# Kernel optimization log

Measured on AMD Instinct MI355X. Metric: run time of the kernel, lower is better.

## Reference

```python
import jax, jax.numpy as jnp
import numpy as np

N = 50000      # nodes
E = 800000     # edges (before self loops)
F_IN = 50      # PPI num_features
H = 4          # heads
C = 64         # hidden per head
NC = 121       # PPI num_classes
NEG_SLOPE = 0.2


def setup_inputs() -> dict:
    key = jax.random.key(0)
    ks = jax.random.split(key, 20)
    p = lambda k, shape: (jax.random.normal(k, shape, jnp.float32) * 0.1)
    x0 = jax.random.normal(ks[0], (N, F_IN), jnp.float32)
    edge_index = jax.random.randint(ks[1], (2, E), 0, N, dtype=jnp.int64)
    return dict(
        x0=x0, edge_index=edge_index,
        W1=p(ks[2], (F_IN, H * C)), as1=p(ks[3], (H, C)), ad1=p(ks[4], (H, C)),
        res1=p(ks[5], (F_IN, H * C)), b1=jnp.zeros((H * C,), jnp.float32),
        W2=p(ks[6], (H * C, H * C)), as2=p(ks[7], (H, C)), ad2=p(ks[8], (H, C)),
        res2=p(ks[9], (H * C, H * C)), b2=jnp.zeros((H * C,), jnp.float32),
        W3=p(ks[10], (H * C, H * NC)), as3=p(ks[11], (H, NC)), ad3=p(ks[12], (H, NC)),
        res3=p(ks[13], (H * C, NC)), b3=jnp.zeros((NC,), jnp.float32),
    )


def _gat(x, src, dst, W, a_src, a_dst, resW, b, concat):
    """PyG-style GATConv with residual, self loops already in (src, dst)."""
    n = x.shape[0]
    heads, outc = a_src.shape
    h = (x @ W).reshape(n, heads, outc)                 # [N,H,C]
    al_s = (h * a_src).sum(-1)                          # [N,H]
    al_d = (h * a_dst).sum(-1)                          # [N,H]
    e = jax.nn.leaky_relu(al_s[src] + al_d[dst], NEG_SLOPE)  # [E,H]
    m = jax.ops.segment_max(e, dst, num_segments=n)     # stable softmax per dst
    ex = jnp.exp(e - m[dst])
    denom = jax.ops.segment_sum(ex, dst, num_segments=n)
    alpha = ex / denom[dst]                             # [E,H]
    out = jax.ops.segment_sum(h[src] * alpha[:, :, None], dst, num_segments=n)  # [N,H,C]
    out = out.reshape(n, heads * outc) if concat else out.mean(axis=1)
    return out + x @ resW + b


def reference(x0, edge_index,
              W1, as1, ad1, res1, b1,
              W2, as2, ad2, res2, b2,
              W3, as3, ad3, res3, b3):
    n = x0.shape[0]
    loop = jnp.arange(n, dtype=edge_index.dtype)        # add self loops (PyG default)
    src = jnp.concatenate([edge_index[0], loop])
    dst = jnp.concatenate([edge_index[1], loop])
    x1 = jax.nn.relu(_gat(x0, src, dst, W1, as1, ad1, res1, b1, True))
    x2 = jax.nn.relu(_gat(x1, src, dst, W2, as2, ad2, res2, b2, True))
    x3 = _gat(x2, src, dst, W3, as3, ad3, res3, b3, False)
    return x3
```

## Files before the change

### kernel.cpp

```cpp
#include <hip/hip_runtime.h>

#define NNODES 50000
#define NEDGES 800000
#define NTOT   (NEDGES + NNODES)
#define F_IN   50
#define KPAD1  64
#define HEADS  4
#define C1     64
#define HC1    256
#define NC     121
#define K1S    320
#define K3S    1280
#define N2S    512

typedef unsigned short ushort_t;
typedef __attribute__((ext_vector_type(4))) unsigned short ushort4_t;
typedef __attribute__((ext_vector_type(8))) unsigned short ushort8;
typedef __attribute__((ext_vector_type(8))) __bf16 bf16x8;
typedef __attribute__((ext_vector_type(4))) float f32x4;
typedef __attribute__((ext_vector_type(4))) int int4_t;

__device__ __forceinline__ ushort_t f2bf(float f) {
    union { float f; unsigned int u; } v; v.f = f;
    unsigned int u = v.u;
    return (ushort_t)((u + 0x7fffu + ((u >> 16) & 1u)) >> 16);
}
__device__ __forceinline__ float bf2f(ushort_t s) {
    union { unsigned int u; float f; } v; v.u = ((unsigned int)s) << 16;
    return v.f;
}
__device__ __forceinline__ float lrelu(float x) { return x > 0.f ? x : 0.2f * x; }
__device__ __forceinline__ f32x4 cvt4(ushort4_t v) {
    f32x4 r; r[0] = bf2f(v.x); r[1] = bf2f(v.y); r[2] = bf2f(v.z); r[3] = bf2f(v.w);
    return r;
}
__device__ __forceinline__ void wave_lds_sync() {
    asm volatile("s_waitcnt lgkmcnt(0)" ::: "memory");
}

__global__ void count_kernel(const int* __restrict__ ei, int* __restrict__ cnt) {
    int i = blockIdx.x * blockDim.x + threadIdx.x;
    if (i >= NTOT) return;
    int d = (i < NEDGES) ? ei[NEDGES + i] : (i - NEDGES);
    if ((unsigned)d >= NNODES) d = 0;
    atomicAdd(&cnt[d], 1);
}

#define SCB 256
__global__ __launch_bounds__(SCB)
void scan1_kernel(const int* __restrict__ cnt, int* __restrict__ incl,
                  int* __restrict__ bsums, int n) {
    __shared__ int buf[SCB];
    int b = blockIdx.x, tid = threadIdx.x;
    int i = b * SCB + tid;
    int v = (i < n) ? cnt[i] : 0;
    buf[tid] = v;
    __syncthreads();
    for (int off = 1; off < SCB; off <<= 1) {
        int t = (tid >= off) ? buf[tid - off] : 0;
        __syncthreads();
        buf[tid] += t;
        __syncthreads();
    }
    if (i < n) incl[i] = buf[tid];
    if (tid == SCB - 1) bsums[b] = buf[tid];
}

__global__ __launch_bounds__(SCB)
void scan2_kernel(int* __restrict__ bsums, int nb) {
    __shared__ int buf[SCB];
    int tid = threadIdx.x;
    int v = (tid < nb) ? bsums[tid] : 0;
    buf[tid] = v;
    __syncthreads();
    for (int off = 1; off < SCB; off <<= 1) {
        int t = (tid >= off) ? buf[tid - off] : 0;
        __syncthreads();
        buf[tid] += t;
        __syncthreads();
    }
    if (tid < nb) bsums[tid] = buf[tid] - v;
}

__global__ __launch_bounds__(SCB)
void scan3_kernel(const int* __restrict__ cnt, const int* __restrict__ incl,
                  const int* __restrict__ bsums, int* __restrict__ row_ptr,
                  int* __restrict__ cursor, int n) {
    int b = blockIdx.x, tid = threadIdx.x;
    int i = b * SCB + tid;
    if (i >= n) return;
    int e = bsums[b] + incl[i] - cnt[i];
    row_ptr[i] = e; cursor[i] = e;
    if (i == n - 1) row_ptr[n] = NTOT;
}

__global__ void scatter_kernel(const int* __restrict__ ei, int* __restrict__ cursor,
                               int* __restrict__ csr_src) {
    int i = blockIdx.x * blockDim.x + threadIdx.x;
    if (i >= NTOT) return;
    int s, d;
    if (i < NEDGES) { s = ei[i]; d = ei[NEDGES + i]; }
    else            { s = d = i - NEDGES; }
    if ((unsigned)d >= NNODES) d = 0;
    if ((unsigned)s >= NNODES) s = 0;
    int pos = atomicAdd(&cursor[d], 1);
    csr_src[pos] = s;
}

#define SZ_A (NNODES * KPAD1)
#define SZ_B (HC1 * K1S)
#define SZ_C (N2S * HC1)
#define SZ_D (N2S)
#define SZ_E (NC * K3S)
#define SZ_F (KPAD1 * 4)
#define SZ_G (HC1 * 4)
#define PREP_TOTAL (SZ_A + SZ_B + SZ_C + SZ_D + SZ_E + 2 * SZ_F + 4 * SZ_G)

__global__ __launch_bounds__(256)
void prep_kernel(const float* __restrict__ x0,
                 const float* __restrict__ W1, const float* __restrict__ res1,
                 const float* __restrict__ W2, const float* __restrict__ res2,
                 const float* __restrict__ W3, const float* __restrict__ res3,
                 const float* __restrict__ as1, const float* __restrict__ ad1,
                 const float* __restrict__ as2, const float* __restrict__ ad2,
                 const float* __restrict__ as3, const float* __restrict__ ad3,
                 const float* __restrict__ b2,
                 ushort_t* __restrict__ x0b, ushort_t* __restrict__ Bt1,
                 ushort_t* __restrict__ Bt2, ushort_t* __restrict__ Bt3,
                 float* __restrict__ bias512,
                 float* __restrict__ w_as1, float* __restrict__ w_ad1,
                 float* __restrict__ w_as2, float* __restrict__ w_ad2,
                 float* __restrict__ w_as3, float* __restrict__ w_ad3) {
    int i = blockIdx.x * 256 + threadIdx.x;
    if (i < SZ_A) {
        int m = i >> 6, k = i & 63;
        x0b[i] = (k < F_IN) ? f2bf(x0[(size_t)m * F_IN + k]) : (ushort_t)0;
        return;
    }
    i -= SZ_A;
    if (i < SZ_B) {
        int c = i / K1S, kk = i - c * K1S;
        float v = 0.f;
        if (kk < 256) {
            int h = kk >> 6, k = kk & 63;
            if (k < F_IN && (c >> 6) == h) v = W1[(size_t)k * HC1 + c];
        } else {
            int k = kk - 256;
            if (k < F_IN) v = res1[(size_t)k * HC1 + c];
        }
        Bt1[i] = f2bf(v);
        return;
    }
    i -= SZ_B;
    if (i < SZ_C) {
        int c = i / HC1, k = i - c * HC1;
        float v = (c < HC1) ? W2[(size_t)k * HC1 + c] : res2[(size_t)k * HC1 + (c - HC1)];
        Bt2[i] = f2bf(v);
        return;
    }
    i -= SZ_C;
    if (i < SZ_D) {
        bias512[i] = (i < HC1) ? 0.f : b2[i - HC1];
        return;
    }
    i -= SZ_D;
    if (i < SZ_E) {
        int c = i / K3S, kk = i - c * K3S;
        float v;
        if (kk < 1024) {
            int h = kk >> 8, k = kk & 255;
            v = 0.25f * W3[(size_t)k * (HEADS * NC) + h * NC + c];
        } else {
            int k = kk - 1024;
            v = res3[(size_t)k * NC + c];
        }
        Bt3[i] = f2bf(v);
        return;
    }
    i -= SZ_E;
    if (i < 2 * SZ_F) {
        const float* a = (i < SZ_F) ? as1 : ad1;
        float* w = (i < SZ_F) ? w_as1 : w_ad1;
        int ii = (i < SZ_F) ? i : i - SZ_F;
        int k = ii >> 2, h = ii & 3;
        float s = 0.f;
        if (k < F_IN)
            for (int c = 0; c < C1; ++c) s += W1[(size_t)k * HC1 + h * C1 + c] * a[h * C1 + c];
        w[ii] = s;
        return;
    }
    i -= 2 * SZ_F;
    {
        int grp = i / SZ_G, ii = i - grp * SZ_G;
        int k = ii >> 2, h = ii & 3;
        float s = 0.f;
        if (grp < 2) {
            const float* a = grp ? ad2 : as2;
            for (int c = 0; c < C1; ++c) s += W2[(size_t)k * HC1 + h * C1 + c] * a[h * C1 + c];
            (grp ? w_ad2 : w_as2)[ii] = s;
        } else {
            const float* a = (grp == 3) ? ad3 : as3;
            for (int c = 0; c < NC; ++c) s += W3[(size_t)k * (HEADS * NC) + h * NC + c] * a[h * NC + c];
            ((grp == 3) ? w_ad3 : w_as3)[ii] = s;
        }
    }
}

#define BM 128
#define BN 128
#define BK 64
#define LDP (BK + 8)

__global__ __launch_bounds__(256)
void gemm_mfma_kernel(const ushort_t* __restrict__ A1, int lda1,
                      const ushort_t* __restrict__ A2, int lda2, int Ksplit,
                      const ushort_t* __restrict__ Bt, const float* __restrict__ bias,
                      float* __restrict__ Cf, ushort_t* __restrict__ Cb,
                      int M, int N, int K, int relu) {
    __shared__ ushort_t As[BM * LDP];
    __shared__ ushort_t Bs[BN * LDP];
    int tid = threadIdx.x;
    int lane = tid & 63;
    int wid = tid >> 6;
    int wm = (wid & 1) * 64, wn = (wid >> 1) * 64;
    int l15 = lane & 15;
    int q8 = (lane >> 4) * 8;
    int m0 = blockIdx.y * BM, n0 = blockIdx.x * BN;

    f32x4 acc[4][4] = {};

    for (int k0 = 0; k0 < K; k0 += BK) {
        #pragma unroll
        for (int it = 0; it < 4; ++it) {
            int c = tid + it * 256;
            int row = c >> 3, c8 = c & 7;
            int k = k0 + c8 * 8;
            ushort8 va = (ushort8)0;
            int gm = m0 + row;
            if (gm < M) {
                if (k < Ksplit) va = *(const ushort8*)&A1[(size_t)gm * lda1 + k];
                else            va = *(const ushort8*)&A2[(size_t)gm * lda2 + (k - Ksplit)];
            }
            *(ushort8*)&As[row * LDP + c8 * 8] = va;
            ushort8 vb = (ushort8)0;
            int gn = n0 + row;
            if (gn < N) vb = *(const ushort8*)&Bt[(size_t)gn * K + k];
            *(ushort8*)&Bs[row * LDP + c8 * 8] = vb;
        }
        __syncthreads();
        #pragma unroll
        for (int kk = 0; kk < BK; kk += 32) {
            bf16x8 af[4], bfr[4];
            #pragma unroll
            for (int mi = 0; mi < 4; ++mi)
                af[mi] = *(const bf16x8*)&As[(wm + mi * 16 + l15) * LDP + kk + q8];
            #pragma unroll
            for (int ni = 0; ni < 4; ++ni)
                bfr[ni] = *(const bf16x8*)&Bs[(wn + ni * 16 + l15) * LDP + kk + q8];
            #pragma unroll
            for (int mi = 0; mi < 4; ++mi)
                #pragma unroll
                for (int ni = 0; ni < 4; ++ni)
                    acc[mi][ni] = __builtin_amdgcn_mfma_f32_16x16x32_bf16(
                        af[mi], bfr[ni], acc[mi][ni], 0, 0, 0);
        }
        __syncthreads();
    }

    #pragma unroll
    for (int mi = 0; mi < 4; ++mi) {
        int mbase = m0 + wm + mi * 16 + (lane >> 4) * 4;
        #pragma unroll
        for (int ni = 0; ni < 4; ++ni) {
            int ncol = n0 + wn + ni * 16 + l15;
            if (ncol >= N) continue;
            float bv = bias ? bias[ncol] : 0.f;
            #pragma unroll
            for (int r = 0; r < 4; ++r) {
                int m = mbase + r;
                if (m >= M) continue;
                float v = acc[mi][ni][r] + bv;
                if (relu) v = fmaxf(v, 0.f);
                if (Cf) Cf[(size_t)m * N + ncol] = v;
                else    Cb[(size_t)m * N + ncol] = f2bf(v);
            }
        }
    }
}

__global__ __launch_bounds__(256)
void logits_gemv_kernel(const ushort_t* __restrict__ X, int K,
                        const float* __restrict__ w_as, const float* __restrict__ w_ad,
                        float* __restrict__ als, float* __restrict__ ald) {
    int wid = threadIdx.x >> 6, lane = threadIdx.x & 63;
    int n = blockIdx.x * 4 + wid;
    float ps[HEADS] = {}, pd[HEADS] = {};
    for (int k0 = lane * 4; k0 < K; k0 += 256) {
        ushort4_t xv = *(const ushort4_t*)&X[(size_t)n * K + k0];
        float x[4] = {bf2f(xv.x), bf2f(xv.y), bf2f(xv.z), bf2f(xv.w)};
        #pragma unroll
        for (int j = 0; j < 4; ++j) {
            #pragma unroll
            for (int h = 0; h < HEADS; ++h) {
                ps[h] += x[j] * w_as[(k0 + j) * 4 + h];
                pd[h] += x[j] * w_ad[(k0 + j) * 4 + h];
            }
        }
    }
    #pragma unroll
    for (int off = 32; off; off >>= 1)
        #pragma unroll
        for (int h = 0; h < HEADS; ++h) {
            ps[h] += __shfl_xor(ps[h], off);
            pd[h] += __shfl_xor(pd[h], off);
        }
    if (lane == 0)
        #pragma unroll
        for (int h = 0; h < HEADS; ++h) {
            als[n * HEADS + h] = ps[h];
            ald[n * HEADS + h] = pd[h];
        }
}

#define E_CHUNK_NOMAX(ROWBYTES)                                               \
    int i = base + lane;                                                      \
    int nv = end - base; if (nv > 64) nv = 64;                                \
    if (i < end) {                                                            \
        int s = csr_src[i];                                                   \
        soffw[lane] = s * (ROWBYTES);                                         \
        f32x4 av = *(const f32x4*)&als[s * 4];                                \
        f32x4 e;                                                              \
        _Pragma("unroll")                                                     \
        for (int h = 0; h < HEADS; ++h) {                                     \
            e[h] = __expf(lrelu(av[h] + aldd[h]));                            \
            den4[h] += e[h];                                                  \
        }                                                                     \
        *(f32x4*)&sew[lane * 4] = e;                                          \
    }                                                                         \
    wave_lds_sync();

#define DEN_REDUCE                                                            \
    _Pragma("unroll")                                                         \
    for (int off = 32; off; off >>= 1)                                        \
        _Pragma("unroll")                                                     \
        for (int h = 0; h < HEADS; ++h)                                       \
            den4[h] += __shfl_xor(den4[h], off);

__global__ __launch_bounds__(256)
void agg1_kernel(const ushort_t* __restrict__ x0b,
                 const float* __restrict__ als, const float* __restrict__ ald,
                 const int* __restrict__ row_ptr, const int* __restrict__ csr_src,
                 ushort_t* __restrict__ aggx) {
    __shared__ int   soff[4][64];
    __shared__ float se[4][64 * 4];
    int wid = threadIdx.x >> 6, lane = threadIdx.x & 63;
    int d = blockIdx.x * 4 + wid;
    int* soffw = soff[wid];
    float* sew = se[wid];
    int beg = row_ptr[d], end = row_ptr[d + 1];
    f32x4 aldd = *(const f32x4*)&ald[d * 4];
    f32x4 den4 = (f32x4)0.f;
    f32x4 acc  = (f32x4)0.f;
    int lb = lane * 2;
    for (int base = beg; base < end; base += 64) {
        E_CHUNK_NOMAX(KPAD1 * 2)
        int j = 0;
        for (; j + 4 <= nv; j += 4) {
            int4_t o = *(const int4_t*)&soffw[j];
            f32x4 e0 = *(const f32x4*)&sew[j * 4];
            f32x4 e1 = *(const f32x4*)&sew[(j + 1) * 4];
            f32x4 e2 = *(const f32x4*)&sew[(j + 2) * 4];
            f32x4 e3 = *(const f32x4*)&sew[(j + 3) * 4];
            float x0v = bf2f(*(const ushort_t*)((const char*)x0b + o.x + lb));
            float x1v = bf2f(*(const ushort_t*)((const char*)x0b + o.y + lb));
            float x2v = bf2f(*(const ushort_t*)((const char*)x0b + o.z + lb));
            float x3v = bf2f(*(const ushort_t*)((const char*)x0b + o.w + lb));
            acc += e0 * x0v + e1 * x1v + e2 * x2v + e3 * x3v;
        }
        for (; j < nv; ++j) {
            int o = soffw[j];
            f32x4 e = *(const f32x4*)&sew[j * 4];
            float xv = bf2f(*(const ushort_t*)((const char*)x0b + o + lb));
            acc += e * xv;
        }
        wave_lds_sync();
    }
    DEN_REDUCE
    #pragma unroll
    for (int h = 0; h < HEADS; ++h)
        aggx[(size_t)d * HC1 + h * 64 + lane] = f2bf(acc[h] / den4[h]);
}

__global__ __launch_bounds__(256)
void agg2_kernel(const ushort_t* __restrict__ comb,
                 const float* __restrict__ als, const float* __restrict__ ald,
                 const int* __restrict__ row_ptr, const int* __restrict__ csr_src,
                 const float* __restrict__ w_as3, const float* __restrict__ w_ad3,
                 ushort_t* __restrict__ xnext,
                 float* __restrict__ als3, float* __restrict__ ald3) {
    __shared__ int   soff[4][64];
    __shared__ float se[4][64 * 4];
    int wid = threadIdx.x >> 6, lane = threadIdx.x & 63;
    int d = blockIdx.x * 4 + wid;
    int* soffw = soff[wid];
    float* sew = se[wid];
    int hh = lane >> 4;
    int beg = row_ptr[d], end = row_ptr[d + 1];
    f32x4 aldd = *(const f32x4*)&ald[d * 4];
    f32x4 den4 = (f32x4)0.f;
    f32x4 acc  = (f32x4)0.f;
    int lb = lane * 8;
    for (int base = beg; base < end; base += 64) {
        E_CHUNK_NOMAX(N2S * 2)
        int j = 0;
        for (; j + 4 <= nv; j += 4) {
            int4_t o = *(const int4_t*)&soffw[j];
            float e0 = sew[j * 4 + hh], e1 = sew[(j + 1) * 4 + hh];
            float e2 = sew[(j + 2) * 4 + hh], e3 = sew[(j + 3) * 4 + hh];
            f32x4 x0v = cvt4(*(const ushort4_t*)((const char*)comb + o.x + lb));
            f32x4 x1v = cvt4(*(const ushort4_t*)((const char*)comb + o.y + lb));
            f32x4 x2v = cvt4(*(const ushort4_t*)((const char*)comb + o.z + lb));
            f32x4 x3v = cvt4(*(const ushort4_t*)((const char*)comb + o.w + lb));
            acc += e0 * x0v + e1 * x1v + e2 * x2v + e3 * x3v;
        }
        for (; j < nv; ++j) {
            int o = soffw[j];
            float e = sew[j * 4 + hh];
            acc += e * cvt4(*(const ushort4_t*)((const char*)comb + o + lb));
        }
        wave_lds_sync();
    }
    DEN_REDUCE
    float r = 1.f / den4[hh];
    ushort4_t rv = *(const ushort4_t*)&comb[(size_t)d * N2S + 256 + lane * 4];
    f32x4 resv = cvt4(rv);
    f32x4 vout;
    #pragma unroll
    for (int c = 0; c < 4; ++c) vout[c] = fmaxf(acc[c] * r + resv[c], 0.f);
    ushort4_t o4;
    o4.x = f2bf(vout[0]); o4.y = f2bf(vout[1]); o4.z = f2bf(vout[2]); o4.w = f2bf(vout[3]);
    *(ushort4_t*)&xnext[(size_t)d * HC1 + lane * 4] = o4;
    f32x4 ps = (f32x4)0.f, pd = (f32x4)0.f;
    #pragma unroll
    for (int j = 0; j < 4; ++j) {
        f32x4 wsj = *(const f32x4*)&w_as3[(lane * 4 + j) * 4];
        f32x4 wdj = *(const f32x4*)&w_ad3[(lane * 4 + j) * 4];
        ps += vout[j] * wsj;
        pd += vout[j] * wdj;
    }
    #pragma unroll
    for (int off = 32; off; off >>= 1) {
        #pragma unroll
        for (int h = 0; h < HEADS; ++h) {
            ps[h] += __shfl_xor(ps[h], off);
            pd[h] += __shfl_xor(pd[h], off);
        }
    }
    if (lane == 0) {
        *(f32x4*)&als3[d * 4] = ps;
        *(f32x4*)&ald3[d * 4] = pd;
    }
}

__global__ __launch_bounds__(256)
void agg3_kernel(const ushort_t* __restrict__ x2b,
                 const float* __restrict__ als, const float* __restrict__ ald,
                 const int* __restrict__ row_ptr, const int* __restrict__ csr_src,
                 ushort_t* __restrict__ aggx) {
    __shared__ int   soff[4][64];
    __shared__ float se[4][64 * 4];
    int wid = threadIdx.x >> 6, lane = threadIdx.x & 63;
    int d = blockIdx.x * 4 + wid;
    int* soffw = soff[wid];
    float* sew = se[wid];
    int beg = row_ptr[d], end = row_ptr[d + 1];
    f32x4 aldd = *(const f32x4*)&ald[d * 4];
    f32x4 den4 = (f32x4)0.f;
    f32x4 acc[HEADS] = {};
    int lb = lane * 8;
    for (int base = beg; base < end; base += 64) {
        E_CHUNK_NOMAX(HC1 * 2)
        int j = 0;
        for (; j + 4 <= nv; j += 4) {
            int4_t o = *(const int4_t*)&soffw[j];
            f32x4 e0 = *(const f32x4*)&sew[j * 4];
            f32x4 e1 = *(const f32x4*)&sew[(j + 1) * 4];
            f32x4 e2 = *(const f32x4*)&sew[(j + 2) * 4];
            f32x4 e3 = *(const f32x4*)&sew[(j + 3) * 4];
            f32x4 x0v = cvt4(*(const ushort4_t*)((const char*)x2b + o.x + lb));
            f32x4 x1v = cvt4(*(const ushort4_t*)((const char*)x2b + o.y + lb));
            f32x4 x2v = cvt4(*(const ushort4_t*)((const char*)x2b + o.z + lb));
            f32x4 x3v = cvt4(*(const ushort4_t*)((const char*)x2b + o.w + lb));
            #pragma unroll
            for (int h = 0; h < HEADS; ++h)
                acc[h] += e0[h] * x0v + e1[h] * x1v + e2[h] * x2v + e3[h] * x3v;
        }
        for (; j < nv; ++j) {
            int o = soffw[j];
            f32x4 e = *(const f32x4*)&sew[j * 4];
            f32x4 xv = cvt4(*(const ushort4_t*)((const char*)x2b + o + lb));
            #pragma unroll
            for (int h = 0; h < HEADS; ++h) acc[h] += e[h] * xv;
        }
        wave_lds_sync();
    }
    DEN_REDUCE
    #pragma unroll
    for (int h = 0; h < HEADS; ++h) {
        float rd = 1.f / den4[h];
        ushort4_t o4;
        o4.x = f2bf(acc[h][0] * rd); o4.y = f2bf(acc[h][1] * rd);
        o4.z = f2bf(acc[h][2] * rd); o4.w = f2bf(acc[h][3] * rd);
        *(ushort4_t*)&aggx[(size_t)d * 1024 + h * HC1 + lane * 4] = o4;
    }
}

extern "C" void kernel_launch(void* const* d_in, const int* in_sizes, int n_in,
                              void* d_out, int out_size, void* d_ws, size_t ws_size,
                              hipStream_t stream) {
    const float* x0   = (const float*)d_in[0];
    const int*   ei   = (const int*)d_in[1];
    const float* W1   = (const float*)d_in[2];
    const float* as1  = (const float*)d_in[3];
    const float* ad1  = (const float*)d_in[4];
    const float* res1 = (const float*)d_in[5];
    const float* b1   = (const float*)d_in[6];
    const float* W2   = (const float*)d_in[7];
    const float* as2  = (const float*)d_in[8];
    const float* ad2  = (const float*)d_in[9];
    const float* res2 = (const float*)d_in[10];
    const float* b2   = (const float*)d_in[11];
    const float* W3   = (const float*)d_in[12];
    const float* as3  = (const float*)d_in[13];
    const float* ad3  = (const float*)d_in[14];
    const float* res3 = (const float*)d_in[15];
    const float* b3   = (const float*)d_in[16];

    char* p = (char*)d_ws;
    auto alloc = [&](size_t bytes) -> void* {
        void* r = (void*)p;
        p += (bytes + 255) & ~(size_t)255;
        return r;
    };
    int*      cnt     = (int*)alloc((size_t)NNODES * 4);
    int*      incl    = (int*)alloc((size_t)NNODES * 4);
    int*      bsums   = (int*)alloc((size_t)SCB * 4);
    int*      row_ptr = (int*)alloc((size_t)(NNODES + 1) * 4);
    int*      cursor  = (int*)alloc((size_t)NNODES * 4);
    int*      csr_src = (int*)alloc((size_t)NTOT * 4);
    float*    als     = (float*)alloc((size_t)NNODES * HEADS * 4);
    float*    ald     = (float*)alloc((size_t)NNODES * HEADS * 4);
    float*    als3    = (float*)alloc((size_t)NNODES * HEADS * 4);
    float*    ald3    = (float*)alloc((size_t)NNODES * HEADS * 4);
    ushort_t* x0b     = (ushort_t*)alloc((size_t)NNODES * KPAD1 * 2);
    ushort_t* x2      = (ushort_t*)alloc((size_t)NNODES * HC1 * 2);
    ushort_t* Bt1     = (ushort_t*)alloc((size_t)HC1 * K1S * 2);
    ushort_t* Bt2     = (ushort_t*)alloc((size_t)N2S * HC1 * 2);
    float*    bias512 = (float*)alloc((size_t)N2S * 4);
    ushort_t* Bt3     = (ushort_t*)alloc((size_t)NC * K3S * 2);
    float*    w_as1   = (float*)alloc((size_t)KPAD1 * 4 * 4);
    float*    w_ad1   = (float*)alloc((size_t)KPAD1 * 4 * 4);
    float*    w_as2   = (float*)alloc((size_t)HC1 * 4 * 4);
    float*    w_ad2   = (float*)alloc((size_t)HC1 * 4 * 4);
    float*    w_as3   = (float*)alloc((size_t)HC1 * 4 * 4);
    float*    w_ad3   = (float*)alloc((size_t)HC1 * 4 * 4);
    char*     big     = (char*)alloc((size_t)NNODES * 1024 * 2);
    ushort_t* aggx1   = (ushort_t*)big;
    ushort_t* x1      = (ushort_t*)(big + (size_t)NNODES * HC1 * 2);
    ushort_t* comb    = (ushort_t*)(big + (size_t)NNODES * HC1 * 4);
    ushort_t* aggx3   = (ushort_t*)big;

    hipMemsetAsync(cnt, 0, (size_t)NNODES * 4, stream);

    int tb = 256;
    int nscan = (NNODES + SCB - 1) / SCB;
    count_kernel<<<(NTOT + tb - 1) / tb, tb, 0, stream>>>(ei, cnt);
    scan1_kernel<<<nscan, SCB, 0, stream>>>(cnt, incl, bsums, NNODES);
    scan2_kernel<<<1, SCB, 0, stream>>>(bsums, nscan);
    scan3_kernel<<<nscan, SCB, 0, stream>>>(cnt, incl, bsums, row_ptr, cursor, NNODES);
    scatter_kernel<<<(NTOT + tb - 1) / tb, tb, 0, stream>>>(ei, cursor, csr_src);

    prep_kernel<<<(PREP_TOTAL + 255) / 256, 256, 0, stream>>>(
        x0, W1, res1, W2, res2, W3, res3, as1, ad1, as2, ad2, as3, ad3, b2,
        x0b, Bt1, Bt2, Bt3, bias512, w_as1, w_ad1, w_as2, w_ad2, w_as3, w_ad3);

    auto gemm = [&](const ushort_t* A1, int lda1, const ushort_t* A2, int lda2, int Ksplit,
                    const ushort_t* Bt, const float* bias,
                    float* Cf, ushort_t* Cb, int M, int Nn, int K, int relu) {
        dim3 g((Nn + BN - 1) / BN, (M + BM - 1) / BM);
        gemm_mfma_kernel<<<g, 256, 0, stream>>>(A1, lda1, A2, lda2, Ksplit, Bt, bias,
                                                Cf, Cb, M, Nn, K, relu);
    };

    int nagg = NNODES / 4;

    logits_gemv_kernel<<<nagg, 256, 0, stream>>>(x0b, KPAD1, w_as1, w_ad1, als, ald);
    agg1_kernel<<<nagg, 256, 0, stream>>>(x0b, als, ald, row_ptr, csr_src, aggx1);
    gemm(aggx1, HC1, x0b, KPAD1, HC1, Bt1, b1, nullptr, x1, NNODES, HC1, K1S, 1);

    gemm(x1, HC1, x1, HC1, HC1, Bt2, bias512, nullptr, comb, NNODES, N2S, HC1, 0);
    logits_gemv_kernel<<<nagg, 256, 0, stream>>>(x1, HC1, w_as2, w_ad2, als, ald);
    agg2_kernel<<<nagg, 256, 0, stream>>>(comb, als, ald, row_ptr, csr_src,
                                          w_as3, w_ad3, x2, als3, ald3);

    agg3_kernel<<<nagg, 256, 0, stream>>>(x2, als3, ald3, row_ptr, csr_src, aggx3);
    gemm(aggx3, 1024, x2, HC1, 1024, Bt3, b3, (float*)d_out, nullptr, NNODES, NC, K3S, 0);
}
```

Baseline: 640.7 us.

## Widen gather loads to 16B in aggregation kernels and fuse prep/count, scatter/gemv launches

The three aggregation kernels now gather neighbour rows with 16-byte loads. Each wave splits into lane groups that handle different edges at the same time, and partial sums are combined with cross-lane shuffles at the end. Tail edges are padded with zero weights so the edge loop runs in fixed steps of eight. Separately, prep is fused with the degree count kernel, and the CSR scatter is fused with the first-layer logits GEMV, cutting two launches. The wider per-lane accumulators and the shuffle reductions add register pressure and extra instructions.

New measurement: 767.4 us. 1.2x slower.

```diff
diff --git a/kernel.cpp b/kernel.cpp
--- a/kernel.cpp
+++ b/kernel.cpp
@@ -30,16 +30,20 @@
     return v.f;
 }
 __device__ __forceinline__ float lrelu(float x) { return x > 0.f ? x : 0.2f * x; }
-__device__ __forceinline__ f32x4 cvt4(ushort4_t v) {
-    f32x4 r; r[0] = bf2f(v.x); r[1] = bf2f(v.y); r[2] = bf2f(v.z); r[3] = bf2f(v.w);
+__device__ __forceinline__ f32x4 cvt4lo(ushort8 v) {
+    f32x4 r; r[0] = bf2f(v[0]); r[1] = bf2f(v[1]); r[2] = bf2f(v[2]); r[3] = bf2f(v[3]);
+    return r;
+}
+__device__ __forceinline__ f32x4 cvt4hi(ushort8 v) {
+    f32x4 r; r[0] = bf2f(v[4]); r[1] = bf2f(v[5]); r[2] = bf2f(v[6]); r[3] = bf2f(v[7]);
     return r;
 }
 __device__ __forceinline__ void wave_lds_sync() {
     asm volatile("s_waitcnt lgkmcnt(0)" ::: "memory");
 }
 
-__global__ void count_kernel(const int* __restrict__ ei, int* __restrict__ cnt) {
-    int i = blockIdx.x * blockDim.x + threadIdx.x;
+__device__ __forceinline__ void count_body(int i, const int* __restrict__ ei,
+                                           int* __restrict__ cnt) {
     if (i >= NTOT) return;
     int d = (i < NEDGES) ? ei[NEDGES + i] : (i - NEDGES);
     if ((unsigned)d >= NNODES) d = 0;
@@ -94,9 +98,9 @@
     if (i == n - 1) row_ptr[n] = NTOT;
 }
 
-__global__ void scatter_kernel(const int* __restrict__ ei, int* __restrict__ cursor,
-                               int* __restrict__ csr_src) {
-    int i = blockIdx.x * blockDim.x + threadIdx.x;
+__device__ __forceinline__ void scatter_body(int i, const int* __restrict__ ei,
+                                             int* __restrict__ cursor,
+                                             int* __restrict__ csr_src) {
     if (i >= NTOT) return;
     int s, d;
     if (i < NEDGES) { s = ei[i]; d = ei[NEDGES + i]; }
@@ -115,9 +119,11 @@
 #define SZ_F (KPAD1 * 4)
 #define SZ_G (HC1 * 4)
 #define PREP_TOTAL (SZ_A + SZ_B + SZ_C + SZ_D + SZ_E + 2 * SZ_F + 4 * SZ_G)
-
-__global__ __launch_bounds__(256)
-void prep_kernel(const float* __restrict__ x0,
+#define PREP_BLK ((PREP_TOTAL + 255) / 256)
+#define CNT_BLK  ((NTOT + 255) / 256)
+
+__device__ void prep_body(int i,
+                 const float* __restrict__ x0,
                  const float* __restrict__ W1, const float* __restrict__ res1,
                  const float* __restrict__ W2, const float* __restrict__ res2,
                  const float* __restrict__ W3, const float* __restrict__ res3,
@@ -131,7 +137,6 @@
                  float* __restrict__ w_as1, float* __restrict__ w_ad1,
                  float* __restrict__ w_as2, float* __restrict__ w_ad2,
                  float* __restrict__ w_as3, float* __restrict__ w_ad3) {
-    int i = blockIdx.x * 256 + threadIdx.x;
     if (i < SZ_A) {
         int m = i >> 6, k = i & 63;
         x0b[i] = (k < F_IN) ? f2bf(x0[(size_t)m * F_IN + k]) : (ushort_t)0;
@@ -203,6 +208,32 @@
             for (int c = 0; c < NC; ++c) s += W3[(size_t)k * (HEADS * NC) + h * NC + c] * a[h * NC + c];
             ((grp == 3) ? w_ad3 : w_as3)[ii] = s;
         }
+    }
+}
+
+__global__ __launch_bounds__(256)
+void prep_count_kernel(const float* __restrict__ x0,
+                 const float* __restrict__ W1, const float* __restrict__ res1,
+                 const float* __restrict__ W2, const float* __restrict__ res2,
+                 const float* __restrict__ W3, const float* __restrict__ res3,
+                 const float* __restrict__ as1, const float* __restrict__ ad1,
+                 const float* __restrict__ as2, const float* __restrict__ ad2,
+                 const float* __restrict__ as3, const float* __restrict__ ad3,
+                 const float* __restrict__ b2,
+                 ushort_t* __restrict__ x0b, ushort_t* __restrict__ Bt1,
+                 ushort_t* __restrict__ Bt2, ushort_t* __restrict__ Bt3,
+                 float* __restrict__ bias512,
+                 float* __restrict__ w_as1, float* __restrict__ w_ad1,
+                 float* __restrict__ w_as2, float* __restrict__ w_ad2,
+                 float* __restrict__ w_as3, float* __restrict__ w_ad3,
+                 const int* __restrict__ ei, int* __restrict__ cnt) {
+    int b = blockIdx.x;
+    if (b < PREP_BLK) {
+        prep_body(b * 256 + threadIdx.x, x0, W1, res1, W2, res2, W3, res3,
+                  as1, ad1, as2, ad2, as3, ad3, b2, x0b, Bt1, Bt2, Bt3,
+                  bias512, w_as1, w_ad1, w_as2, w_ad2, w_as3, w_ad3);
+    } else {
+        count_body((b - PREP_BLK) * 256 + threadIdx.x, ei, cnt);
     }
 }
 
@@ -288,43 +319,64 @@
     }
 }
 
+__device__ __forceinline__ void gemv_body(int n, int lane,
+                        const ushort_t* __restrict__ X, int K,
+                        const float* __restrict__ w_as, const float* __restrict__ w_ad,
+                        float* __restrict__ als, float* __restrict__ ald) {
+    float ps[HEADS] = {}, pd[HEADS] = {};
+    for (int k0 = lane * 4; k0 < K; k0 += 256) {
+        ushort4_t xv = *(const ushort4_t*)&X[(size_t)n * K + k0];
+        float x[4] = {bf2f(xv.x), bf2f(xv.y), bf2f(xv.z), bf2f(xv.w)};
+        #pragma unroll
+        for (int j = 0; j < 4; ++j) {
+            #pragma unroll
+            for (int h = 0; h < HEADS; ++h) {
+                ps[h] += x[j] * w_as[(k0 + j) * 4 + h];
+                pd[h] += x[j] * w_ad[(k0 + j) * 4 + h];
+            }
+        }
+    }
+    #pragma unroll
+    for (int off = 32; off; off >>= 1)
+        #pragma unroll
+        for (int h = 0; h < HEADS; ++h) {
+            ps[h] += __shfl_xor(ps[h], off);
+            pd[h] += __shfl_xor(pd[h], off);
+        }
+    if (lane == 0)
+        #pragma unroll
+        for (int h = 0; h < HEADS; ++h) {
+            als[n * HEADS + h] = ps[h];
+            ald[n * HEADS + h] = pd[h];
+        }
+}
+
 __global__ __launch_bounds__(256)
 void logits_gemv_kernel(const ushort_t* __restrict__ X, int K,
                         const float* __restrict__ w_as, const float* __restrict__ w_ad,
                         float* __restrict__ als, float* __restrict__ ald) {
-    int wid = threadIdx.x >> 6, lane = threadIdx.x & 63;
-    int n = blockIdx.x * 4 + wid;
-    float ps[HEADS] = {}, pd[HEADS] = {};
-    for (int k0 = lane * 4; k0 < K; k0 += 256) {
-        ushort4_t xv = *(const ushort4_t*)&X[(size_t)n * K + k0];
-        float x[4] = {bf2f(xv.x), bf2f(xv.y), bf2f(xv.z), bf2f(xv.w)};
-        #pragma unroll
-        for (int j = 0; j < 4; ++j) {
-            #pragma unroll
-            for (int h = 0; h < HEADS; ++h) {
-                ps[h] += x[j] * w_as[(k0 + j) * 4 + h];
-                pd[h] += x[j] * w_ad[(k0 + j) * 4 + h];
-            }
-        }
-    }
-    #pragma unroll
-    for (int off = 32; off; off >>= 1)
-        #pragma unroll
-        for (int h = 0; h < HEADS; ++h) {
-            ps[h] += __shfl_xor(ps[h], off);
-            pd[h] += __shfl_xor(pd[h], off);
-        }
-    if (lane == 0)
-        #pragma unroll
-        for (int h = 0; h < HEADS; ++h) {
-            als[n * HEADS + h] = ps[h];
-            ald[n * HEADS + h] = pd[h];
-        }
+    gemv_body(blockIdx.x * 4 + (threadIdx.x >> 6), threadIdx.x & 63, X, K, w_as, w_ad, als, ald);
+}
+
+#define GEMV_BLK (NNODES / 4)
+__global__ __launch_bounds__(256)
+void scatter_gemv1_kernel(const int* __restrict__ ei, int* __restrict__ cursor,
+                          int* __restrict__ csr_src,
+                          const ushort_t* __restrict__ X,
+                          const float* __restrict__ w_as, const float* __restrict__ w_ad,
+                          float* __restrict__ als, float* __restrict__ ald) {
+    int b = blockIdx.x;
+    if (b < GEMV_BLK) {
+        gemv_body(b * 4 + (threadIdx.x >> 6), threadIdx.x & 63, X, KPAD1, w_as, w_ad, als, ald);
+    } else {
+        scatter_body((b - GEMV_BLK) * 256 + threadIdx.x, ei, cursor, csr_src);
+    }
 }
 
 #define E_CHUNK_NOMAX(ROWBYTES)                                               \
     int i = base + lane;                                                      \
     int nv = end - base; if (nv > 64) nv = 64;                                \
+    int nv8 = (nv + 7) & ~7;                                                  \
     if (i < end) {                                                            \
         int s = csr_src[i];                                                   \
         soffw[lane] = s * (ROWBYTES);                                         \
@@ -336,6 +388,9 @@
             den4[h] += e[h];                                                  \
         }                                                                     \
         *(f32x4*)&sew[lane * 4] = e;                                          \
+    } else {                                                                  \
+        soffw[lane] = 0;                                                      \
+        *(f32x4*)&sew[lane * 4] = (f32x4)0.f;                                 \
     }                                                                         \
     wave_lds_sync();
 
@@ -357,38 +412,48 @@
     int d = blockIdx.x * 4 + wid;
     int* soffw = soff[wid];
     float* sew = se[wid];
+    int g  = lane >> 3;
+    int cl = lane & 7;
+    int lb = cl * 16;
     int beg = row_ptr[d], end = row_ptr[d + 1];
     f32x4 aldd = *(const f32x4*)&ald[d * 4];
     f32x4 den4 = (f32x4)0.f;
-    f32x4 acc  = (f32x4)0.f;
-    int lb = lane * 2;
+    f32x4 acc[HEADS][2] = {};
     for (int base = beg; base < end; base += 64) {
         E_CHUNK_NOMAX(KPAD1 * 2)
-        int j = 0;
-        for (; j + 4 <= nv; j += 4) {
-            int4_t o = *(const int4_t*)&soffw[j];
-            f32x4 e0 = *(const f32x4*)&sew[j * 4];
-            f32x4 e1 = *(const f32x4*)&sew[(j + 1) * 4];
-            f32x4 e2 = *(const f32x4*)&sew[(j + 2) * 4];
-            f32x4 e3 = *(const f32x4*)&sew[(j + 3) * 4];
-            float x0v = bf2f(*(const ushort_t*)((const char*)x0b + o.x + lb));
-            float x1v = bf2f(*(const ushort_t*)((const char*)x0b + o.y + lb));
-            float x2v = bf2f(*(const ushort_t*)((const char*)x0b + o.z + lb));
-            float x3v = bf2f(*(const ushort_t*)((const char*)x0b + o.w + lb));
-            acc += e0 * x0v + e1 * x1v + e2 * x2v + e3 * x3v;
-        }
-        for (; j < nv; ++j) {
-            int o = soffw[j];
-            f32x4 e = *(const f32x4*)&sew[j * 4];
-            float xv = bf2f(*(const ushort_t*)((const char*)x0b + o + lb));
-            acc += e * xv;
+        for (int j = 0; j < nv8; j += 8) {
+            int o = soffw[j + g];
+            f32x4 e = *(const f32x4*)&sew[(j + g) * 4];
+            ushort8 v = *(const ushort8*)((const char*)x0b + o + lb);
+            f32x4 xl = cvt4lo(v), xh = cvt4hi(v);
+            #pragma unroll
+            for (int h = 0; h < HEADS; ++h) {
+                acc[h][0] += e[h] * xl;
+                acc[h][1] += e[h] * xh;
+            }
         }
         wave_lds_sync();
     }
     DEN_REDUCE
     #pragma unroll
-    for (int h = 0; h < HEADS; ++h)
-        aggx[(size_t)d * HC1 + h * 64 + lane] = f2bf(acc[h] / den4[h]);
+    for (int off = 8; off <= 32; off <<= 1)
+        #pragma unroll
+        for (int h = 0; h < HEADS; ++h)
+            #pragma unroll
+            for (int q = 0; q < 2; ++q)
+                #pragma unroll
+                for (int c = 0; c < 4; ++c)
+                    acc[h][q][c] += __shfl_xor(acc[h][q][c], off);
+    if (g < 4) {
+        float rdv = 1.f / den4[g];
+        ushort8 ow;
+        #pragma unroll
+        for (int q = 0; q < 2; ++q)
+            #pragma unroll
+            for (int c = 0; c < 4; ++c)
+                ow[q * 4 + c] = f2bf(acc[g][q][c] * rdv);
+        *(ushort8*)&aggx[(size_t)d * HC1 + g * 64 + cl * 8] = ow;
+    }
 }
 
 __global__ __launch_bounds__(256)
@@ -404,49 +469,60 @@
     int d = blockIdx.x * 4 + wid;
     int* soffw = soff[wid];
     float* sew = se[wid];
-    int hh = lane >> 4;
+    int p4 = (lane >> 5) * 4;
+    int cl = lane & 31;
+    int hl = cl >> 3;
+    int lb = cl * 16;
     int beg = row_ptr[d], end = row_ptr[d + 1];
     f32x4 aldd = *(const f32x4*)&ald[d * 4];
     f32x4 den4 = (f32x4)0.f;
-    f32x4 acc  = (f32x4)0.f;
-    int lb = lane * 8;
+    f32x4 acc[2] = {};
     for (int base = beg; base < end; base += 64) {
         E_CHUNK_NOMAX(N2S * 2)
-        int j = 0;
-        for (; j + 4 <= nv; j += 4) {
-            int4_t o = *(const int4_t*)&soffw[j];
-            float e0 = sew[j * 4 + hh], e1 = sew[(j + 1) * 4 + hh];
-            float e2 = sew[(j + 2) * 4 + hh], e3 = sew[(j + 3) * 4 + hh];
-            f32x4 x0v = cvt4(*(const ushort4_t*)((const char*)comb + o.x + lb));
-            f32x4 x1v = cvt4(*(const ushort4_t*)((const char*)comb + o.y + lb));
-            f32x4 x2v = cvt4(*(const ushort4_t*)((const char*)comb + o.z + lb));
-            f32x4 x3v = cvt4(*(const ushort4_t*)((const char*)comb + o.w + lb));
-            acc += e0 * x0v + e1 * x1v + e2 * x2v + e3 * x3v;
-        }
-        for (; j < nv; ++j) {
-            int o = soffw[j];
-            float e = sew[j * 4 + hh];
-            acc += e * cvt4(*(const ushort4_t*)((const char*)comb + o + lb));
+        for (int j = 0; j < nv8; j += 8) {
+            int4_t o = *(const int4_t*)&soffw[j + p4];
+            ushort8 v0 = *(const ushort8*)((const char*)comb + o.x + lb);
+            ushort8 v1 = *(const ushort8*)((const char*)comb + o.y + lb);
+            ushort8 v2 = *(const ushort8*)((const char*)comb + o.z + lb);
+            ushort8 v3 = *(const ushort8*)((const char*)comb + o.w + lb);
+            float e0 = sew[(j + p4 + 0) * 4 + hl];
+            float e1 = sew[(j + p4 + 1) * 4 + hl];
+            float e2 = sew[(j + p4 + 2) * 4 + hl];
+            float e3 = sew[(j + p4 + 3) * 4 + hl];
+            acc[0] += e0 * cvt4lo(v0) + e1 * cvt4lo(v1) + e2 * cvt4lo(v2) + e3 * cvt4lo(v3);
+            acc[1] += e0 * cvt4hi(v0) + e1 * cvt4hi(v1) + e2 * cvt4hi(v2) + e3 * cvt4hi(v3);
         }
         wave_lds_sync();
     }
     DEN_REDUCE
-    float r = 1.f / den4[hh];
-    ushort4_t rv = *(const ushort4_t*)&comb[(size_t)d * N2S + 256 + lane * 4];
-    f32x4 resv = cvt4(rv);
-    f32x4 vout;
     #pragma unroll
-    for (int c = 0; c < 4; ++c) vout[c] = fmaxf(acc[c] * r + resv[c], 0.f);
-    ushort4_t o4;
-    o4.x = f2bf(vout[0]); o4.y = f2bf(vout[1]); o4.z = f2bf(vout[2]); o4.w = f2bf(vout[3]);
-    *(ushort4_t*)&xnext[(size_t)d * HC1 + lane * 4] = o4;
+    for (int q = 0; q < 2; ++q)
+        #pragma unroll
+        for (int c = 0; c < 4; ++c)
+            acc[q][c] += __shfl_xor(acc[q][c], 32);
     f32x4 ps = (f32x4)0.f, pd = (f32x4)0.f;
-    #pragma unroll
-    for (int j = 0; j < 4; ++j) {
-        f32x4 wsj = *(const f32x4*)&w_as3[(lane * 4 + j) * 4];
-        f32x4 wdj = *(const f32x4*)&w_ad3[(lane * 4 + j) * 4];
-        ps += vout[j] * wsj;
-        pd += vout[j] * wdj;
+    if (lane < 32) {
+        float r = 1.f / den4[hl];
+        ushort8 rv = *(const ushort8*)&comb[(size_t)d * N2S + 256 + cl * 8];
+        float vout[8];
+        ushort8 o8;
+        #pragma unroll
+        for (int q = 0; q < 2; ++q)
+            #pragma unroll
+            for (int c = 0; c < 4; ++c) {
+                float vv = fmaxf(acc[q][c] * r + bf2f(rv[q * 4 + c]), 0.f);
+                vout[q * 4 + c] = vv;
+                o8[q * 4 + c] = f2bf(vv);
+            }
+        *(ushort8*)&xnext[(size_t)d * HC1 + cl * 8] = o8;
+        #pragma unroll
+        for (int cc = 0; cc < 8; ++cc) {
+            int col = cl * 8 + cc;
+            f32x4 wsj = *(const f32x4*)&w_as3[col * 4];
+            f32x4 wdj = *(const f32x4*)&w_ad3[col * 4];
+            ps += vout[cc] * wsj;
+            pd += vout[cc] * wdj;
+        }
     }
     #pragma unroll
     for (int off = 32; off; off >>= 1) {
@@ -473,45 +549,61 @@
     int d = blockIdx.x * 4 + wid;
     int* soffw = soff[wid];
     float* sew = se[wid];
+    int p4 = (lane >> 5) * 4;
+    int cl = lane & 31;
+    int lb = cl * 16;
     int beg = row_ptr[d], end = row_ptr[d + 1];
     f32x4 aldd = *(const f32x4*)&ald[d * 4];
     f32x4 den4 = (f32x4)0.f;
-    f32x4 acc[HEADS] = {};
-    int lb = lane * 8;
+    f32x4 acc[HEADS][2] = {};
     for (int base = beg; base < end; base += 64) {
         E_CHUNK_NOMAX(HC1 * 2)
-        int j = 0;
-        for (; j + 4 <= nv; j += 4) {
-            int4_t o = *(const int4_t*)&soffw[j];
-            f32x4 e0 = *(const f32x4*)&sew[j * 4];
-            f32x4 e1 = *(const f32x4*)&sew[(j + 1) * 4];
-            f32x4 e2 = *(const f32x4*)&sew[(j + 2) * 4];
-            f32x4 e3 = *(const f32x4*)&sew[(j + 3) * 4];
-            f32x4 x0v = cvt4(*(const ushort4_t*)((const char*)x2b + o.x + lb));
-            f32x4 x1v = cvt4(*(const ushort4_t*)((const char*)x2b + o.y + lb));
-            f32x4 x2v = cvt4(*(const ushort4_t*)((const char*)x2b + o.z + lb));
-            f32x4 x3v = cvt4(*(const ushort4_t*)((const char*)x2b + o.w + lb));
-            #pragma unroll
-            for (int h = 0; h < HEADS; ++h)
-                acc[h] += e0[h] * x0v + e1[h] * x1v + e2[h] * x2v + e3[h] * x3v;
-        }
-        for (; j < nv; ++j) {
-            int o = soffw[j];
-            f32x4 e = *(const f32x4*)&sew[j * 4];
-            f32x4 xv = cvt4(*(const ushort4_t*)((const char*)x2b + o + lb));
-            #pragma unroll
-            for (int h = 0; h < HEADS; ++h) acc[h] += e[h] * xv;
+        for (int j = 0; j < nv8; j += 8) {
+            int4_t o = *(const int4_t*)&soffw[j + p4];
+            ushort8 v0 = *(const ushort8*)((const char*)x2b + o.x + lb);
+            ushort8 v1 = *(const ushort8*)((const char*)x2b + o.y + lb);
+            ushort8 v2 = *(const ushort8*)((const char*)x2b + o.z + lb);
+            ushort8 v3 = *(const ushort8*)((const char*)x2b + o.w + lb);
+            f32x4 e0 = *(const f32x4*)&sew[(j + p4 + 0) * 4];
+            f32x4 e1 = *(const f32x4*)&sew[(j + p4 + 1) * 4];
+            f32x4 e2 = *(const f32x4*)&sew[(j + p4 + 2) * 4];
+            f32x4 e3 = *(const f32x4*)&sew[(j + p4 + 3) * 4];
+            f32x4 xl, xh;
+            xl = cvt4lo(v0); xh = cvt4hi(v0);
+            #pragma unroll
+            for (int h = 0; h < HEADS; ++h) { acc[h][0] += e0[h] * xl; acc[h][1] += e0[h] * xh; }
+            xl = cvt4lo(v1); xh = cvt4hi(v1);
+            #pragma unroll
+            for (int h = 0; h < HEADS; ++h) { acc[h][0] += e1[h] * xl; acc[h][1] += e1[h] * xh; }
+            xl = cvt4lo(v2); xh = cvt4hi(v2);
+            #pragma unroll
+            for (int h = 0; h < HEADS; ++h) { acc[h][0] += e2[h] * xl; acc[h][1] += e2[h] * xh; }
+            xl = cvt4lo(v3); xh = cvt4hi(v3);
+            #pragma unroll
+            for (int h = 0; h < HEADS; ++h) { acc[h][0] += e3[h] * xl; acc[h][1] += e3[h] * xh; }
         }
         wave_lds_sync();
     }
     DEN_REDUCE
     #pragma unroll
-    for (int h = 0; h < HEADS; ++h) {
-        float rd = 1.f / den4[h];
-        ushort4_t o4;
-        o4.x = f2bf(acc[h][0] * rd); o4.y = f2bf(acc[h][1] * rd);
-        o4.z = f2bf(acc[h][2] * rd); o4.w = f2bf(acc[h][3] * rd);
-        *(ushort4_t*)&aggx[(size_t)d * 1024 + h * HC1 + lane * 4] = o4;
+    for (int h = 0; h < HEADS; ++h)
+        #pragma unroll
+        for (int q = 0; q < 2; ++q)
+            #pragma unroll
+            for (int c = 0; c < 4; ++c)
+                acc[h][q][c] += __shfl_xor(acc[h][q][c], 32);
+    int hbase = (lane >> 5) * 2;
+    #pragma unroll
+    for (int hh = 0; hh < 2; ++hh) {
+        int h = hbase + hh;
+        float rdv = 1.f / den4[h];
+        ushort8 ow;
+        #pragma unroll
+        for (int q = 0; q < 2; ++q)
+            #pragma unroll
+            for (int c = 0; c < 4; ++c)
+                ow[q * 4 + c] = f2bf(acc[h][q][c] * rdv);
+        *(ushort8*)&aggx[(size_t)d * 1024 + h * HC1 + cl * 8] = ow;
     }
 }
 
@@ -572,17 +664,17 @@
 
     hipMemsetAsync(cnt, 0, (size_t)NNODES * 4, stream);
 
-    int tb = 256;
     int nscan = (NNODES + SCB - 1) / SCB;
-    count_kernel<<<(NTOT + tb - 1) / tb, tb, 0, stream>>>(ei, cnt);
+
+    prep_count_kernel<<<PREP_BLK + CNT_BLK, 256, 0, stream>>>(
+        x0, W1, res1, W2, res2, W3, res3, as1, ad1, as2, ad2, as3, ad3, b2,
+        x0b, Bt1, Bt2, Bt3, bias512, w_as1, w_ad1, w_as2, w_ad2, w_as3, w_ad3,
+        ei, cnt);
     scan1_kernel<<<nscan, SCB, 0, stream>>>(cnt, incl, bsums, NNODES);
     scan2_kernel<<<1, SCB, 0, stream>>>(bsums, nscan);
     scan3_kernel<<<nscan, SCB, 0, stream>>>(cnt, incl, bsums, row_ptr, cursor, NNODES);
-    scatter_kernel<<<(NTOT + tb - 1) / tb, tb, 0, stream>>>(ei, cursor, csr_src);
-
-    prep_kernel<<<(PREP_TOTAL + 255) / 256, 256, 0, stream>>>(
-        x0, W1, res1, W2, res2, W3, res3, as1, ad1, as2, ad2, as3, ad3, b2,
-        x0b, Bt1, Bt2, Bt3, bias512, w_as1, w_ad1, w_as2, w_ad2, w_as3, w_ad3);
+    scatter_gemv1_kernel<<<GEMV_BLK + CNT_BLK, 256, 0, stream>>>(
+        ei, cursor, csr_src, x0b, w_as1, w_ad1, als, ald);
 
     auto gemm = [&](const ushort_t* A1, int lda1, const ushort_t* A2, int lda2, int Ksplit,
                     const ushort_t* Bt, const float* bias,
@@ -594,7 +686,6 @@
 
     int nagg = NNODES / 4;
 
-    logits_gemv_kernel<<<nagg, 256, 0, stream>>>(x0b, KPAD1, w_as1, w_ad1, als, ald);
     agg1_kernel<<<nagg, 256, 0, stream>>>(x0b, als, ald, row_ptr, csr_src, aggx1);
     gemm(aggx1, HC1, x0b, KPAD1, HC1, Bt1, b1, nullptr, x1, NNODES, HC1, K1S, 1);
 
```
